# Kernel optimization log

Measured on AMD Instinct MI355X. Metric: run time of the kernel, lower is better.

The kernel has to match this reference:

```python
import jax, jax.numpy as jnp
import numpy as np

N = 6144      # nodes
DIN = 65      # input_dim (1 time + 64 space coords)
DOUT = 65     # output_dim per head
H = 4         # nheads
EPS = 1e-7
MIN = 1e-15
# curvature c = 1 throughout (MultiHeadGraphAttentionLayer hardcodes curvature=1)

def arcosh(z):
    return jnp.log(z + jnp.sqrt(jnp.maximum(z * z - 1.0, 0.0)))

def hyp_proj(u):
    # project onto hyperboloid: recompute time coord
    y = u[..., 1:]
    t = jnp.sqrt(1.0 + jnp.sum(y * y, -1, keepdims=True))
    return jnp.concatenate([t, y], -1)

def expmap0(u):
    v = u[..., 1:]
    n = jnp.maximum(jnp.linalg.norm(v, axis=-1, keepdims=True), MIN)
    return jnp.concatenate([jnp.cosh(n), jnp.sinh(n) * v / n], -1)

def logmap0(x):
    y = x[..., 1:]
    n = jnp.maximum(jnp.linalg.norm(y, axis=-1, keepdims=True), MIN)
    t = jnp.maximum(x[..., :1], 1.0 + EPS)
    return jnp.concatenate([jnp.zeros_like(t), arcosh(t) * y / n], -1)

def hyp_linear(x, W):
    # HypLinear (use_bias=False, eval mode): mobius_matvec = exp0(log0(x) @ W^T), then proj
    return hyp_proj(expmap0(logmap0(x) @ W.T))

def to_poincare(x):
    return x[..., 1:] / (x[..., :1] + 1.0)

def to_hyperboloid(p):
    s = jnp.sum(p * p, -1, keepdims=True)
    return jnp.concatenate([1.0 + s, 2.0 * p], -1) / jnp.maximum(1.0 - s, MIN)

def mobius_half(v):
    # 0.5 (x) v  (mobius scalar multiplication, c=1)
    n = jnp.maximum(jnp.linalg.norm(v, axis=-1, keepdims=True), MIN)
    return jnp.tanh(0.5 * jnp.arctanh(jnp.minimum(n, 1.0 - EPS))) * v / n

def head(x, adj_t, Wa, Wd, Wo):
    att = hyp_linear(x, Wa)   # [N, DOUT]
    red = hyp_linear(x, Wd)   # [N, DOUT]
    # pairwise hyperboloid sqdist via Minkowski inner product (negate time coord)
    am = att.at[:, 0].multiply(-1.0)
    theta = jnp.maximum(-(am @ att.T), 1.0 + EPS)          # [N, N]
    S = jnp.minimum(arcosh(theta) ** 2, 50.0)
    # coef[i, j] = -adj[j, i] * sqdist for incoming edges (mask = adj^T)
    coef = jnp.where(adj_t > 0.01, -adj_t * S, 0.0)
    # F.normalize along incoming-edge axis (zeros don't change the L2 norm)
    a = coef / jnp.maximum(jnp.linalg.norm(coef, axis=-1, keepdims=True), 1e-12)
    pv = to_poincare(red)                                   # [N, DOUT-1]
    lam = 2.0 / jnp.maximum(1.0 - jnp.sum(pv * pv, -1), MIN)  # conformal factors [N]
    num = (a * lam[None, :]) @ pv                           # [N, DOUT-1]
    den = jnp.sum(jnp.abs(a) * (lam - 1.0)[None, :], -1, keepdims=True)
    m = mobius_half(num / jnp.maximum(den, MIN))            # mobius midpoint
    return hyp_linear(to_hyperboloid(m), Wo)                # [N, DOUT]

def reference(x, adj, W_att, W_data, W_out, W_lin):
    adj_t = adj.T
    hs = jnp.stack([head(x, adj_t, W_att[h], W_data[h], W_out[h]) for h in range(H)], axis=1)  # [N, H, DOUT]
    p = to_poincare(hs).reshape(x.shape[0], -1)             # PoincareBall.concat -> [N, H*(DOUT-1)]
    return hyp_linear(to_hyperboloid(p), W_lin)             # [N, H*DOUT]

def setup_inputs():
    key = jax.random.key(0)
    ks = jax.random.split(key, 8)
    sp = 0.1 * jax.random.normal(ks[0], (N, DIN - 1), jnp.float32)
    x = jnp.concatenate([jnp.sqrt(1.0 + jnp.sum(sp * sp, -1, keepdims=True)), sp], -1)
    adj = (jax.random.uniform(ks[1], (N, N)) < 32.0 / N).astype(jnp.float32)
    adj = jnp.maximum(adj, jnp.eye(N, dtype=jnp.float32))  # every node >=1 incoming edge
    def xavier(k, shape):
        b = (6.0 / (shape[0] + shape[1])) ** 0.5
        return jax.random.uniform(k, shape, jnp.float32, -b, b)
    W_att = jnp.stack([xavier(jax.random.fold_in(ks[2], h), (DOUT, DIN)) for h in range(H)])
    W_data = jnp.stack([xavier(jax.random.fold_in(ks[3], h), (DOUT, DIN)) for h in range(H)])
    W_out = jnp.stack([xavier(jax.random.fold_in(ks[4], h), (DOUT, DOUT)) for h in range(H)])
    W_lin = xavier(ks[5], (H * DOUT, H * (DOUT - 1) + 1))
    return {"x": x, "adj": adj, "W_att": W_att, "W_data": W_data, "W_out": W_out, "W_lin": W_lin}
```

## Files before the change

### kernel.cpp

```cpp
#include <hip/hip_runtime.h>
#include <hip/hip_fp16.h>
#include <math.h>

#define N 6144
#define H 4
#define CAP 128
#define MINF 1e-15f
#define ONE_EPS  1.0000001192092896f
#define ONE_MEPS 0.9999998807907104f

__device__ __forceinline__ float wave_reduce_sum(float v) {
    v += __shfl_xor(v, 32, 64);
    v += __shfl_xor(v, 16, 64);
    v += __shfl_xor(v, 8, 64);
    v += __shfl_xor(v, 4, 64);
    v += __shfl_xor(v, 2, 64);
    v += __shfl_xor(v, 1, 64);
    return v;
}

__device__ __forceinline__ float arcosh_f(float z) {
    return logf(z + sqrtf(fmaxf(z * z - 1.0f, 0.0f)));
}

__device__ __forceinline__ void h8_to_f(float4 r, float* o) {
    __half2* h = (__half2*)&r;
    #pragma unroll
    for (int q = 0; q < 4; q++) {
        float2 f = __half22float2(h[q]);
        o[2 * q + 0] = f.x;
        o[2 * q + 1] = f.y;
    }
}

__device__ __forceinline__ int bitrev4(int t) {
    return ((t & 1) << 3) | ((t & 2) << 1) | ((t & 4) >> 1) | ((t & 8) >> 3);
}

__global__ void k_prep(const float* __restrict__ x, float* __restrict__ lmv,
                       const float* __restrict__ W_att, const float* __restrict__ W_data,
                       const float* __restrict__ W_out, const float* __restrict__ Wl,
                       float* __restrict__ Bp, float* __restrict__ Bo,
                       float* __restrict__ WlT, int* __restrict__ cnt) {
    int b = blockIdx.x;
    if (b < 1536) {
        int i = b * 4 + (threadIdx.x >> 6);
        int lane = threadIdx.x & 63;
        float y = x[i * 65 + 1 + lane];
        float ss = wave_reduce_sum(y * y);
        float n = fmaxf(sqrtf(ss), MINF);
        float t = fmaxf(x[i * 65], ONE_EPS);
        lmv[i * 64 + lane] = arcosh_f(t) * y / n;
    } else if (b < 1728) {
        int tid = (b - 1536) * 256 + threadIdx.x;
        int m = tid >> 12;
        int r = tid & 4095;
        int k = r >> 6, o = r & 63;
        const float* src;
        if (m < 4) src = W_att + m * 65 * 65;
        else if (m < 8) src = W_data + (m - 4) * 65 * 65;
        else src = W_out + (m - 8) * 65 * 65;
        if (m < 8) {
            Bp[m * 4096 + k * 64 + o] = src[(1 + o) * 65 + (1 + k)];
        } else {
            int dk = (k & 3) * 16 + bitrev4(k >> 2);
            Bo[(m - 8) * 4096 + k * 64 + o] = src[(1 + o) * 65 + (1 + dk)];
        }
    } else if (b < 1808) {
        int L = ((b - 1728) * 256 + threadIdx.x) * 4;
        int k = L / 320, o0 = L % 320;
        float v[4];
        #pragma unroll
        for (int q = 0; q < 4; q++) {
            int o = o0 + q;
            v[q] = (o < 259) ? Wl[(size_t)(1 + o) * 257 + 1 + k] : 0.f;
        }
        *(float4*)(WlT + L) = make_float4(v[0], v[1], v[2], v[3]);
    } else {
        cnt[(b - 1808) * 256 + threadIdx.x] = 0;
    }
}

__global__ void __launch_bounds__(256) k_csr_gemm(
        const float* __restrict__ adj, int* __restrict__ cnt, int* __restrict__ idx,
        const float* __restrict__ lmv, const float* __restrict__ Bp,
        __half* __restrict__ kv, float2* __restrict__ a0l) {
    __shared__ float smem[64 * 65];
    if (blockIdx.x < 768) {
        float (*As)[64] = (float(*)[64])smem;
        float (*Bs)[64] = (float(*)[64])(smem + 1024);
        float (*Cs)[65] = (float(*)[65])smem;
        int my = blockIdx.x / 96;
        int ix = blockIdx.x % 96;
        const float* Bb = Bp + (size_t)my * 4096;
        int i0 = ix * 64;
        int tid = threadIdx.x;
        int tx = tid & 15, ty = tid >> 4;
        float acc[4][4] = {};
        for (int k0 = 0; k0 < 64; k0 += 16) {
            {
                int mm = tid >> 2, kq = tid & 3;
                float4 v = *(const float4*)(lmv + (size_t)(i0 + mm) * 64 + k0 + kq * 4);
                As[kq * 4 + 0][mm] = v.x;
                As[kq * 4 + 1][mm] = v.y;
                As[kq * 4 + 2][mm] = v.z;
                As[kq * 4 + 3][mm] = v.w;
            }
            {
                int kk = tid >> 4, o4 = tid & 15;
                float4 bvv = *(const float4*)(Bb + (k0 + kk) * 64 + o4 * 4);
                *(float4*)&Bs[kk][o4 * 4] = bvv;
            }
            __syncthreads();
            #pragma unroll
            for (int kk = 0; kk < 16; kk++) {
                float4 av = *(const float4*)&As[kk][ty * 4];
                float4 bv = *(const float4*)&Bs[kk][tx * 4];
                float a[4] = {av.x, av.y, av.z, av.w};
                float b[4] = {bv.x, bv.y, bv.z, bv.w};
                #pragma unroll
                for (int r = 0; r < 4; r++)
                    #pragma unroll
                    for (int c = 0; c < 4; c++) acc[r][c] += a[r] * b[c];
            }
            __syncthreads();
        }
        #pragma unroll
        for (int r = 0; r < 4; r++)
            #pragma unroll
            for (int c = 0; c < 4; c++)
                Cs[ty * 4 + r][tx * 4 + c] = acc[r][c];
        __syncthreads();
        int w = tid >> 6, lane = tid & 63;
        bool isAtt = my < 4;
        int h = my & 3;
        #pragma unroll 1
        for (int r = 0; r < 16; r++) {
            int row = w * 16 + r;
            int i = i0 + row;
            float u = Cs[row][lane];
            float nn = fmaxf(sqrtf(wave_reduce_sum(u * u)), MINF);
            if (isAtt) {
                float sha = sinhf(nn);
                kv[((size_t)h * N + i) * 128 + lane] = __float2half(sha * u / nn);
                if (lane == 0) a0l[h * N + i].x = coshf(nn);
            } else {
                float shd = sinhf(nn), chd = coshf(nn);
                float pvd = (shd * u / nn) / (chd + 1.0f);
                kv[((size_t)h * N + i) * 128 + 64 + lane] = __float2half(pvd);
                float sp = wave_reduce_sum(pvd * pvd);
                if (lane == 0) a0l[h * N + i].y = 2.0f / fmaxf(1.0f - sp, MINF);
            }
        }
    } else {
        const uint4* a4 = (const uint4*)adj;
        unsigned sb = blockIdx.x - 768;
        unsigned base4 = sb * 2304u + (unsigned)threadIdx.x;
        unsigned s0 = 0, s1 = 0, s2 = 0, s3 = 0;
        int ns = 0;
        uint4 v0 = a4[base4];
        uint4 v1 = a4[base4 + 256u];
        uint4 v2 = a4[base4 + 512u];
        uint4 v3 = a4[base4 + 768u];
        #pragma unroll
        for (int it = 0; it < 9; it++) {
            uint4 u = (it & 3) == 0 ? v0 : (it & 3) == 1 ? v1
                    : (it & 3) == 2 ? v2 : v3;
            if (it + 4 < 9) {
                uint4 nv = a4[base4 + (unsigned)(it + 4) * 256u];
                if ((it & 3) == 0) v0 = nv;
                else if ((it & 3) == 1) v1 = nv;
                else if ((it & 3) == 2) v2 = nv;
                else v3 = nv;
            }
            if (u.x | u.y | u.z | u.w) {
                unsigned uu[4] = {u.x, u.y, u.z, u.w};
                #pragma unroll
                for (int q = 0; q < 4; q++) {
                    if (uu[q]) {
                        unsigned code = (unsigned)(it * 4 + q);
                        if (ns == 0) s0 = code;
                        else if (ns == 1) s1 = code;
                        else if (ns == 2) s2 = code;
                        else if (ns == 3) s3 = code;
                        else {
                            unsigned t = (base4 + (unsigned)it * 256u) * 4u + q;
                            int j = t / N;
                            int i = t % N;
                            int pos = atomicAdd(&cnt[i], 1);
                            if (pos < CAP) idx[i * CAP + pos] = j;
                        }
                        ns++;
                    }
                }
            }
        }
        #pragma unroll
        for (int k = 0; k < 4; k++) {
            if (ns > k) {
                unsigned code = (k == 0) ? s0 : (k == 1) ? s1 : (k == 2) ? s2 : s3;
                unsigned it = code >> 2, q = code & 3;
                unsigned t = (base4 + it * 256u) * 4u + q;
                int j = t / N;
                int i = t % N;
                int pos = atomicAdd(&cnt[i], 1);
                if (pos < CAP) idx[i * CAP + pos] = j;
            }
        }
    }
}

__global__ void __launch_bounds__(256) k_attn(
        const int* __restrict__ cnt, const int* __restrict__ idx,
        const __half* __restrict__ kv, const float2* __restrict__ a0l,
        float* __restrict__ lm2) {
    int w = threadIdx.x >> 6, lane = threadIdx.x & 63;
    int gb = blockIdx.x;
    int slot = gb & 7;
    int h = slot >> 1;
    int iblk = (gb >> 3) * 2 + (slot & 1);
    int i = iblk * 4 + w;

    const __half* kvh = kv + (size_t)h * N * 128;
    const float2* a0lh = a0l + (size_t)h * N;
    int c = lane & 3, t = lane >> 2;

    float ai[16];
    {
        float4 r0 = *(const float4*)(kvh + (size_t)i * 128 + c * 16);
        float4 r1 = *(const float4*)(kvh + (size_t)i * 128 + c * 16 + 8);
        h8_to_f(r0, ai);
        h8_to_f(r1, ai + 8);
    }
    float ai0 = a0lh[i].x;
    int nn = min(cnt[i], CAP);

    float accd = 0.f, accss = 0.f;
    float accn16[16] = {};
    for (int base = 0; base < nn; base += 16) {
        int tt = base + t;
        bool act = tt < nn;
        int j = act ? idx[i * CAP + tt] : i;
        float2 al = a0lh[j];
        const __half* row = kvh + (size_t)j * 128;
        float4 b0 = *(const float4*)(row + c * 16);
        float4 b1 = *(const float4*)(row + c * 16 + 8);
        float4 p0 = *(const float4*)(row + 64 + c * 16);
        float4 p1 = *(const float4*)(row + 64 + c * 16 + 8);
        float bv[16], pw[16];
        h8_to_f(b0, bv);
        h8_to_f(b1, bv + 8);
        h8_to_f(p0, pw);
        h8_to_f(p1, pw + 8);
        float d = 0.f;
        #pragma unroll
        for (int k = 0; k < 16; k++) d += ai[k] * bv[k];
        d += __shfl_xor(d, 1, 64);
        d += __shfl_xor(d, 2, 64);
        float theta = fmaxf(ai0 * al.x - d, ONE_EPS);
        float ar = arcosh_f(theta);
        float S = fminf(ar * ar, 50.0f);
        if (!act || j == i) S = 0.f;
        float wq = S * al.y;
        if (c == 0) {
            accd += S * (al.y - 1.0f);
            accss += S * S;
        }
        #pragma unroll
        for (int k = 0; k < 16; k++) accn16[k] = fmaf(wq, pw[k], accn16[k]);
    }
    accd = wave_reduce_sum(accd);
    accss = wave_reduce_sum(accss);
    float nrm = fmaxf(sqrtf(accss), 1e-12f);
    float den = fmaxf(accd / nrm, MINF);
    float scl = 1.0f / (nrm * den);

    float r8[8];
    {
        bool b0 = t & 1;
        #pragma unroll
        for (int kk = 0; kk < 8; kk++) {
            float mine = b0 ? accn16[kk + 8] : accn16[kk];
            float send = b0 ? accn16[kk] : accn16[kk + 8];
            r8[kk] = mine + __shfl_xor(send, 4, 64);
        }
    }
    float r4[4];
    {
        bool b1 = t & 2;
        #pragma unroll
        for (int kk = 0; kk < 4; kk++) {
            float mine = b1 ? r8[kk + 4] : r8[kk];
            float send = b1 ? r8[kk] : r8[kk + 4];
            r4[kk] = mine + __shfl_xor(send, 8, 64);
        }
    }
    float r2[2];
    {
        bool b2 = t & 4;
        #pragma unroll
        for (int kk = 0; kk < 2; kk++) {
            float mine = b2 ? r4[kk + 2] : r4[kk];
            float send = b2 ? r4[kk] : r4[kk + 2];
            r2[kk] = mine + __shfl_xor(send, 16, 64);
        }
    }
    float r1;
    {
        bool b3 = t & 8;
        float mine = b3 ? r2[1] : r2[0];
        float send = b3 ? r2[0] : r2[1];
        r1 = mine + __shfl_xor(send, 32, 64);
    }

    float v = -scl * r1;
    float nv = fmaxf(sqrtf(wave_reduce_sum(v * v)), MINF);
    float nc = fminf(nv, ONE_MEPS);
    float mh = tanhf(0.5f * atanhf(nc));
    float md = mh * v / nv;
    float s = wave_reduce_sum(md * md);
    float Dh = fmaxf(1.0f - s, MINF);
    float hb0 = (1.0f + s) / Dh;
    float hbv = 2.0f * md / Dh;
    float nh = fmaxf(2.0f * sqrtf(s) / Dh, MINF);
    float t2 = fmaxf(hb0, ONE_EPS);
    lm2[((size_t)h * N + i) * 64 + lane] = arcosh_f(t2) * hbv / nh;
}

#define PS 272
#define BS5 336
__global__ void __launch_bounds__(256) k_tail(
        const float* __restrict__ lm2, const float* __restrict__ Bo,
        const float* __restrict__ WlT, float* __restrict__ out) {
    __shared__ float smem[5376 + 16 * PS];
    float* As1 = smem;
    float* Bs1 = smem + 1088;
    float* Bs5 = smem;
    float* P   = smem + 5376;

    int i0 = blockIdx.x * 16;
    int tid = threadIdx.x;
    int ty = tid >> 4;
    int tx = tid & 15;

    for (int h = 0; h < H; h++) {
        {
            float4 v = *(const float4*)(lm2 + ((size_t)h * N + i0 + ty) * 64 + tx * 4);
            *(float4*)(As1 + ty * 68 + tx * 4) = v;
        }
        float acc[4] = {0.f, 0.f, 0.f, 0.f};
        for (int k0 = 0; k0 < 64; k0 += 16) {
            {
                *(float4*)(Bs1 + ty * 64 + tx * 4) =
                    *(const float4*)(Bo + (size_t)h * 4096 + (k0 + ty) * 64 + tx * 4);
            }
            __syncthreads();
            #pragma unroll
            for (int kk = 0; kk < 16; kk++) {
                float a = As1[ty * 68 + k0 + kk];
                float4 bv = *(const float4*)(Bs1 + kk * 64 + tx * 4);
                acc[0] += a * bv.x;
                acc[1] += a * bv.y;
                acc[2] += a * bv.z;
                acc[3] += a * bv.w;
            }
            __syncthreads();
        }
        float ss = acc[0] * acc[0] + acc[1] * acc[1] + acc[2] * acc[2] + acc[3] * acc[3];
        ss += __shfl_xor(ss, 1, 64);
        ss += __shfl_xor(ss, 2, 64);
        ss += __shfl_xor(ss, 4, 64);
        ss += __shfl_xor(ss, 8, 64);
        float nn = fmaxf(sqrtf(ss), MINF);
        float sh = sinhf(nn), ch = coshf(nn);
        float* Pr = P + ty * PS + h * 64 + tx * 4;
        Pr[0] = (sh * acc[0] / nn) / (ch + 1.0f);
        Pr[1] = (sh * acc[1] / nn) / (ch + 1.0f);
        Pr[2] = (sh * acc[2] / nn) / (ch + 1.0f);
        Pr[3] = (sh * acc[3] / nn) / (ch + 1.0f);
    }
    __syncthreads();

    {
        float sp = 0.f;
        float4 pl[4];
        #pragma unroll
        for (int q = 0; q < 4; q++) {
            pl[q] = *(const float4*)(P + ty * PS + q * 64 + tx * 4);
            sp += pl[q].x * pl[q].x + pl[q].y * pl[q].y
                + pl[q].z * pl[q].z + pl[q].w * pl[q].w;
        }
        sp += __shfl_xor(sp, 1, 64);
        sp += __shfl_xor(sp, 2, 64);
        sp += __shfl_xor(sp, 4, 64);
        sp += __shfl_xor(sp, 8, 64);
        float Dh = fmaxf(1.0f - sp, MINF);
        float t2 = fmaxf((1.0f + sp) / Dh, ONE_EPS);
        float nh = fmaxf(2.0f * sqrtf(sp) / Dh, MINF);
        float ar2 = arcosh_f(t2);
        #pragma unroll
        for (int q = 0; q < 4; q++) {
            float4 v = pl[q];
            v.x = ar2 * (2.0f * v.x / Dh) / nh;
            v.y = ar2 * (2.0f * v.y / Dh) / nh;
            v.z = ar2 * (2.0f * v.z / Dh) / nh;
            v.w = ar2 * (2.0f * v.w / Dh) / nh;
            *(float4*)(P + ty * PS + q * 64 + tx * 4) = v;
        }
    }
    __syncthreads();

    float acc2[5][4] = {};
    for (int k0 = 0; k0 < 256; k0 += 16) {
        {
            #pragma unroll
            for (int q = 0; q < 5; q++)
                *(float4*)(Bs5 + ty * BS5 + q * 64 + tx * 4) =
                    *(const float4*)(WlT + (size_t)(k0 + ty) * 320 + q * 64 + tx * 4);
        }
        __syncthreads();
        #pragma unroll
        for (int kq = 0; kq < 4; kq++) {
            float4 pv4 = *(const float4*)(P + ty * PS + k0 + kq * 4);
            float av[4] = {pv4.x, pv4.y, pv4.z, pv4.w};
            #pragma unroll
            for (int j = 0; j < 4; j++) {
                float a = av[j];
                int kk = kq * 4 + j;
                #pragma unroll
                for (int q = 0; q < 5; q++) {
                    float4 bv = *(const float4*)(Bs5 + kk * BS5 + q * 64 + tx * 4);
                    acc2[q][0] += a * bv.x;
                    acc2[q][1] += a * bv.y;
                    acc2[q][2] += a * bv.z;
                    acc2[q][3] += a * bv.w;
                }
            }
        }
        __syncthreads();
    }

    float ss2 = 0.f;
    #pragma unroll
    for (int q = 0; q < 5; q++)
        ss2 += acc2[q][0] * acc2[q][0] + acc2[q][1] * acc2[q][1]
             + acc2[q][2] * acc2[q][2] + acc2[q][3] * acc2[q][3];
    ss2 += __shfl_xor(ss2, 1, 64);
    ss2 += __shfl_xor(ss2, 2, 64);
    ss2 += __shfl_xor(ss2, 4, 64);
    ss2 += __shfl_xor(ss2, 8, 64);
    float nv = fmaxf(sqrtf(ss2), MINF);
    float sh2 = sinhf(nv);
    float scale = sh2 / nv;
    size_t ob = (size_t)(i0 + ty) * 260;
    #pragma unroll
    for (int q = 0; q < 4; q++) {
        int o = q * 64 + tx * 4;
        out[ob + 1 + o + 0] = scale * acc2[q][0];
        out[ob + 1 + o + 1] = scale * acc2[q][1];
        out[ob + 1 + o + 2] = scale * acc2[q][2];
        out[ob + 1 + o + 3] = scale * acc2[q][3];
    }
    if (tx == 0) {
        out[ob] = sqrtf(1.0f + sh2 * sh2);
        out[ob + 257] = scale * acc2[4][0];
        out[ob + 258] = scale * acc2[4][1];
        out[ob + 259] = scale * acc2[4][2];
    }
}

extern "C" void kernel_launch(void* const* d_in, const int* in_sizes, int n_in,
                              void* d_out, int out_size, void* d_ws, size_t ws_size,
                              hipStream_t stream) {
    const float* x = (const float*)d_in[0];
    const float* adj = (const float*)d_in[1];
    const float* W_att = (const float*)d_in[2];
    const float* W_data = (const float*)d_in[3];
    const float* W_out = (const float*)d_in[4];
    const float* W_lin = (const float*)d_in[5];
    float* out = (float*)d_out;

    char* ws = (char*)d_ws;
    size_t off = 0;
    auto alloc = [&](size_t bytes) {
        void* ptr = ws + off;
        off += (bytes + 255) & ~(size_t)255;
        return ptr;
    };
    int* cnt = (int*)alloc((size_t)N * 4);
    int* idx = (int*)alloc((size_t)N * CAP * 4);
    float* lmv = (float*)alloc((size_t)N * 64 * 4);
    __half* kv = (__half*)alloc((size_t)H * N * 128 * 2);
    float2* a0l = (float2*)alloc((size_t)H * N * 8);
    float* lm2 = (float*)alloc((size_t)H * N * 64 * 4);
    float* Bp = (float*)alloc((size_t)8 * 4096 * 4);
    float* Bo = (float*)alloc((size_t)4 * 4096 * 4);
    float* WlT = (float*)alloc((size_t)256 * 320 * 4);

    k_prep<<<1832, 256, 0, stream>>>(x, lmv, W_att, W_data, W_out, W_lin,
                                     Bp, Bo, WlT, cnt);
    k_csr_gemm<<<4864, 256, 0, stream>>>(adj, cnt, idx, lmv, Bp, kv, a0l);
    k_attn<<<6144, 256, 0, stream>>>(cnt, idx, kv, a0l, lm2);
    k_tail<<<N / 16, 256, 0, stream>>>(lm2, Bo, WlT, out);
}
```

Before: 304.9 us.

## Split adjacency scan into separate kernel with packed per-thread hit records

The dense adjacency scan moves out of the fused CSR+GEMM kernel into its own k_scan1 kernel. That kernel packs up to eight nonzero positions per thread into a 64-bit record and does the atomics for any overflow itself. The fused kernel then reads only these small records to emit the remaining atomic inserts, instead of streaming the 150MB adjacency matrix. This adds a kernel launch and an 8MB record round trip, and it serializes the scan ahead of the GEMM blocks where the two used to run concurrently.

```diff
diff --git a/kernel.cpp b/kernel.cpp
--- a/kernel.cpp
+++ b/kernel.cpp
@@ -81,8 +81,54 @@
     }
 }
 
+__global__ void __launch_bounds__(256) k_scan1(
+        const uint4* __restrict__ a4, uint2* __restrict__ rec,
+        int* __restrict__ cnt, int* __restrict__ idx) {
+    unsigned sb = blockIdx.x;
+    unsigned base4 = sb * 2304u + (unsigned)threadIdx.x;
+    unsigned lo = 0, hi = 0;
+    int ns = 0;
+    uint4 v0 = a4[base4];
+    uint4 v1 = a4[base4 + 256u];
+    uint4 v2 = a4[base4 + 512u];
+    uint4 v3 = a4[base4 + 768u];
+    #pragma unroll
+    for (int it = 0; it < 9; it++) {
+        uint4 u = (it & 3) == 0 ? v0 : (it & 3) == 1 ? v1
+                : (it & 3) == 2 ? v2 : v3;
+        if (it + 4 < 9) {
+            uint4 nv = a4[base4 + (unsigned)(it + 4) * 256u];
+            if ((it & 3) == 0) v0 = nv;
+            else if ((it & 3) == 1) v1 = nv;
+            else if ((it & 3) == 2) v2 = nv;
+            else v3 = nv;
+        }
+        if (u.x | u.y | u.z | u.w) {
+            unsigned uu[4] = {u.x, u.y, u.z, u.w};
+            #pragma unroll
+            for (int q = 0; q < 4; q++) {
+                if (uu[q]) {
+                    unsigned code = (unsigned)(it * 4 + q);
+                    if (ns < 5) lo |= code << (6 * ns);
+                    else if (ns < 8) hi |= code << (6 * (ns - 5));
+                    else {
+                        unsigned t = (base4 + (unsigned)it * 256u) * 4u + q;
+                        int j = t / N;
+                        int i = t % N;
+                        int pos = atomicAdd(&cnt[i], 1);
+                        if (pos < CAP) idx[i * CAP + pos] = j;
+                    }
+                    ns++;
+                }
+            }
+        }
+    }
+    hi |= (unsigned)min(ns, 8) << 24;
+    rec[sb * 256u + threadIdx.x] = make_uint2(lo, hi);
+}
+
 __global__ void __launch_bounds__(256) k_csr_gemm(
-        const float* __restrict__ adj, int* __restrict__ cnt, int* __restrict__ idx,
+        const uint2* __restrict__ rec, int* __restrict__ cnt, int* __restrict__ idx,
         const float* __restrict__ lmv, const float* __restrict__ Bp,
         __half* __restrict__ kv, float2* __restrict__ a0l) {
     __shared__ float smem[64 * 65];
@@ -153,58 +199,24 @@
             }
         }
     } else {
-        const uint4* a4 = (const uint4*)adj;
         unsigned sb = blockIdx.x - 768;
-        unsigned base4 = sb * 2304u + (unsigned)threadIdx.x;
-        unsigned s0 = 0, s1 = 0, s2 = 0, s3 = 0;
-        int ns = 0;
-        uint4 v0 = a4[base4];
-        uint4 v1 = a4[base4 + 256u];
-        uint4 v2 = a4[base4 + 512u];
-        uint4 v3 = a4[base4 + 768u];
-        #pragma unroll
-        for (int it = 0; it < 9; it++) {
-            uint4 u = (it & 3) == 0 ? v0 : (it & 3) == 1 ? v1
-                    : (it & 3) == 2 ? v2 : v3;
-            if (it + 4 < 9) {
-                uint4 nv = a4[base4 + (unsigned)(it + 4) * 256u];
-                if ((it & 3) == 0) v0 = nv;
-                else if ((it & 3) == 1) v1 = nv;
-                else if ((it & 3) == 2) v2 = nv;
-                else v3 = nv;
-            }
-            if (u.x | u.y | u.z | u.w) {
-                unsigned uu[4] = {u.x, u.y, u.z, u.w};
-                #pragma unroll
-                for (int q = 0; q < 4; q++) {
-                    if (uu[q]) {
-                        unsigned code = (unsigned)(it * 4 + q);
-                        if (ns == 0) s0 = code;
-                        else if (ns == 1) s1 = code;
-                        else if (ns == 2) s2 = code;
-                        else if (ns == 3) s3 = code;
-                        else {
-                            unsigned t = (base4 + (unsigned)it * 256u) * 4u + q;
-                            int j = t / N;
-                            int i = t % N;
-                            int pos = atomicAdd(&cnt[i], 1);
-                            if (pos < CAP) idx[i * CAP + pos] = j;
-                        }
-                        ns++;
-                    }
+        unsigned r = sb * 256u + (unsigned)threadIdx.x;
+        uint2 rc = rec[r];
+        int ns = (int)(rc.y >> 24);
+        if (ns) {
+            unsigned base4 = sb * 2304u + (unsigned)threadIdx.x;
+            #pragma unroll
+            for (int k = 0; k < 8; k++) {
+                if (k < ns) {
+                    unsigned code = (k < 5) ? ((rc.x >> (6 * k)) & 63u)
+                                            : ((rc.y >> (6 * (k - 5))) & 63u);
+                    unsigned it = code >> 2, q = code & 3;
+                    unsigned t = (base4 + it * 256u) * 4u + q;
+                    int j = t / N;
+                    int i = t % N;
+                    int pos = atomicAdd(&cnt[i], 1);
+                    if (pos < CAP) idx[i * CAP + pos] = j;
                 }
-            }
-        }
-        #pragma unroll
-        for (int k = 0; k < 4; k++) {
-            if (ns > k) {
-                unsigned code = (k == 0) ? s0 : (k == 1) ? s1 : (k == 2) ? s2 : s3;
-                unsigned it = code >> 2, q = code & 3;
-                unsigned t = (base4 + it * 256u) * 4u + q;
-                int j = t / N;
-                int i = t % N;
-                int pos = atomicAdd(&cnt[i], 1);
-                if (pos < CAP) idx[i * CAP + pos] = j;
             }
         }
     }
@@ -489,6 +501,7 @@
     };
     int* cnt = (int*)alloc((size_t)N * 4);
     int* idx = (int*)alloc((size_t)N * CAP * 4);
+    uint2* rec = (uint2*)alloc((size_t)4096 * 256 * 8);
     float* lmv = (float*)alloc((size_t)N * 64 * 4);
     __half* kv = (__half*)alloc((size_t)H * N * 128 * 2);
     float2* a0l = (float2*)alloc((size_t)H * N * 8);
@@ -499,7 +512,8 @@
 
     k_prep<<<1832, 256, 0, stream>>>(x, lmv, W_att, W_data, W_out, W_lin,
                                      Bp, Bo, WlT, cnt);
-    k_csr_gemm<<<4864, 256, 0, stream>>>(adj, cnt, idx, lmv, Bp, kv, a0l);
+    k_scan1<<<4096, 256, 0, stream>>>((const uint4*)adj, rec, cnt, idx);
+    k_csr_gemm<<<4864, 256, 0, stream>>>(rec, cnt, idx, lmv, Bp, kv, a0l);
     k_attn<<<6144, 256, 0, stream>>>(cnt, idx, kv, a0l, lm2);
     k_tail<<<N / 16, 256, 0, stream>>>(lm2, Bo, WlT, out);
 }
```

New measurement: 333.7 us. 9.4% more time.
